# Performance work log

Measured on AMD Instinct MI355X. Metric: run time of the kernel, lower is better.

The kernel has to match this reference:

```python
import jax, jax.numpy as jnp
import numpy as np

N, M, D = 8192, 8192, 256

def setup_inputs() -> dict:
    key = jax.random.key(0)
    ks = jax.random.split(key, 8)
    s = 1.0 / np.sqrt(D)
    return {
        "x_q": jax.random.normal(ks[0], (N, D), dtype=jnp.float32),
        "x_kv": jax.random.normal(ks[1], (M, D), dtype=jnp.float32),
        "Wq": jax.random.uniform(ks[2], (D, D), minval=-s, maxval=s, dtype=jnp.float32),
        "bq": jax.random.uniform(ks[3], (D,), minval=-s, maxval=s, dtype=jnp.float32),
        "Wk": jax.random.uniform(ks[4], (D, D), minval=-s, maxval=s, dtype=jnp.float32),
        "bk": jax.random.uniform(ks[5], (D,), minval=-s, maxval=s, dtype=jnp.float32),
        "Wv": jax.random.uniform(ks[6], (D, D), minval=-s, maxval=s, dtype=jnp.float32),
        "bv": jax.random.uniform(ks[7], (D,), minval=-s, maxval=s, dtype=jnp.float32),
    }

def reference(x_q, x_kv, Wq, bq, Wk, bk, Wv, bv):
    # Linear layers: y = x @ W^T + b (torch convention: W is [out, in])
    q = x_q @ Wq.T + bq          # [N, D]
    k = x_kv @ Wk.T + bk         # [M, D]
    v = x_kv @ Wv.T + bv         # [M, D]
    scale = jnp.sqrt(jnp.asarray(q.shape[1], q.dtype))
    attn = jnp.einsum('nd,md->nm', q, k) / scale  # [N, M]
    attn = jax.nn.softmax(attn, axis=1)
    return attn @ v              # [N, D]
```

## Files before the change

### kernel.cpp

```cpp
#include <hip/hip_runtime.h>

#define NN 8192
#define MM 8192
#define DD 256
#define NPART 8
#define MPART (MM / NPART)
#define BK 64
#define NT (MPART / BK)
#define QT 32

#define SCALE_C 0.0901684403f
#define RAW_THR 127.5f

typedef short bf16x8 __attribute__((ext_vector_type(8)));
typedef float f32x4 __attribute__((ext_vector_type(4)));
typedef float f32x16 __attribute__((ext_vector_type(16)));
typedef unsigned int u32;
typedef u32 u32x2 __attribute__((ext_vector_type(2)));
typedef u32 u32x4 __attribute__((ext_vector_type(4)));

#define GLL16(src, dst) __builtin_amdgcn_global_load_lds( \
    (__attribute__((address_space(1))) void*)(src), \
    (__attribute__((address_space(3))) void*)(dst), 16, 0, 0)

static __device__ __forceinline__ unsigned char f2fp8(float a) {
    u32 r;
    asm("v_cvt_pk_fp8_f32 %0, %1, %1" : "=v"(r) : "v"(a));
    return (unsigned char)(r & 0xFFu);
}

static __device__ __forceinline__ u32 cvtpk(float lo, float hi) {
    u32 r;
    asm("v_cvt_pk_bf16_f32 %0, %1, %2" : "=v"(r) : "v"(lo), "v"(hi));
    return r;
}

static __device__ __forceinline__ float bf2f(short s) {
    return __builtin_bit_cast(float, (u32)((unsigned short)s) << 16);
}

__global__ __launch_bounds__(256, 2) void proj_kernel(
    const float* __restrict__ xq, const float* __restrict__ xkv,
    const float* __restrict__ Wq, const float* __restrict__ bq,
    const float* __restrict__ Wk, const float* __restrict__ bk,
    const float* __restrict__ Wv, const float* __restrict__ bv,
    unsigned char* __restrict__ q8, unsigned char* __restrict__ k8,
    short* __restrict__ vp)
{
    __shared__ short Xs[64][264];
    __shared__ short Ws[64][264];

    const int bid = blockIdx.x;
    const int iskv = bid >> 9;
    const int t = bid & 511;
    const int rt = t >> 2;
    const int ct = t & 3;
    const float* __restrict__ X = iskv ? xkv : xq;
    const float* __restrict__ W1 = iskv ? Wk : Wq;

    const int tid = threadIdx.x;
    const int lane = tid & 63;
    const int wv = tid >> 6;
    const int l15 = lane & 15;
    const int lg = lane >> 4;

    #pragma unroll
    for (int i = 0; i < 16; ++i) {
        int c = i * 256 + tid;
        int row = c >> 6;
        int col4 = (c & 63) << 2;
        f32x4 xv = *reinterpret_cast<const f32x4*>(X + (size_t)(rt * 64 + row) * DD + col4);
        f32x4 wr = *reinterpret_cast<const f32x4*>(W1 + (size_t)(ct * 64 + row) * DD + col4);
        u32x2 xb, wb;
        xb[0] = cvtpk(xv[0], xv[1]); xb[1] = cvtpk(xv[2], xv[3]);
        wb[0] = cvtpk(wr[0], wr[1]); wb[1] = cvtpk(wr[2], wr[3]);
        *reinterpret_cast<u32x2*>(&Xs[row][col4]) = xb;
        *reinterpret_cast<u32x2*>(&Ws[row][col4]) = wb;
    }
    __syncthreads();

    f32x4 acc[4];
    #pragma unroll
    for (int f = 0; f < 4; ++f) acc[f] = f32x4{0.f, 0.f, 0.f, 0.f};

    #pragma unroll
    for (int kk = 0; kk < 8; ++kk) {
        bf16x8 a = *reinterpret_cast<const bf16x8*>(&Xs[wv * 16 + l15][kk * 32 + lg * 8]);
        #pragma unroll
        for (int f = 0; f < 4; ++f) {
            bf16x8 b = *reinterpret_cast<const bf16x8*>(&Ws[f * 16 + l15][kk * 32 + lg * 8]);
            acc[f] = __builtin_amdgcn_mfma_f32_16x16x32_bf16(a, b, acc[f], 0, 0, 0);
        }
    }

    if (!iskv) {
        #pragma unroll
        for (int f = 0; f < 4; ++f) {
            const int o = ct * 64 + f * 16 + l15;
            const float bsv = bq[o];
            #pragma unroll
            for (int r = 0; r < 4; ++r) {
                const int rowg = rt * 64 + wv * 16 + lg * 4 + r;
                q8[(size_t)rowg * DD + o] = f2fp8(acc[f][r] + bsv);
            }
        }
        return;
    }

    #pragma unroll
    for (int f = 0; f < 4; ++f) {
        const int o = ct * 64 + f * 16 + l15;
        const float bsv = bk[o];
        #pragma unroll
        for (int r = 0; r < 4; ++r) {
            const int rowg = rt * 64 + wv * 16 + lg * 4 + r;
            k8[(size_t)(o >> 3) * (MM * 8) + (size_t)rowg * 8 + (o & 7)] = f2fp8(acc[f][r] + bsv);
        }
    }

    __syncthreads();
    #pragma unroll
    for (int i = 0; i < 16; ++i) {
        int c = i * 256 + tid;
        int row = c >> 6;
        int col4 = (c & 63) << 2;
        f32x4 wr = *reinterpret_cast<const f32x4*>(Wv + (size_t)(ct * 64 + row) * DD + col4);
        u32x2 wb;
        wb[0] = cvtpk(wr[0], wr[1]); wb[1] = cvtpk(wr[2], wr[3]);
        *reinterpret_cast<u32x2*>(&Ws[row][col4]) = wb;
    }
    __syncthreads();

    #pragma unroll
    for (int f = 0; f < 4; ++f) acc[f] = f32x4{0.f, 0.f, 0.f, 0.f};
    #pragma unroll
    for (int kk = 0; kk < 8; ++kk) {
        bf16x8 a = *reinterpret_cast<const bf16x8*>(&Xs[wv * 16 + l15][kk * 32 + lg * 8]);
        #pragma unroll
        for (int f = 0; f < 4; ++f) {
            bf16x8 b = *reinterpret_cast<const bf16x8*>(&Ws[f * 16 + l15][kk * 32 + lg * 8]);
            acc[f] = __builtin_amdgcn_mfma_f32_16x16x32_bf16(a, b, acc[f], 0, 0, 0);
        }
    }
    #pragma unroll
    for (int f = 0; f < 4; ++f) {
        const int o = ct * 64 + f * 16 + l15;
        const float bsv = bv[o];
        const int mb = rt * 64 + wv * 16 + lg * 4;
        u32 w0 = cvtpk(acc[f][0] + bsv, acc[f][1] + bsv);
        u32 w1 = cvtpk(acc[f][2] + bsv, acc[f][3] + bsv);
        u32x2 pk; pk[0] = w0; pk[1] = w1;
        *reinterpret_cast<u32x2*>(&vp[(size_t)(mb >> 6) * 16384 + o * 64 + (mb & 63)]) = pk;
    }
}

__global__ __launch_bounds__(512, 2) void attn_kernel(
    const unsigned char* __restrict__ qg, const unsigned char* __restrict__ kg,
    const short* __restrict__ vp, short* __restrict__ outpB,
    float* __restrict__ statm, float* __restrict__ statl)
{
    extern __shared__ short lds[];
    short* KsBase = lds;
    short* VsBase = lds + 3 * 8192;

    const int bid = blockIdx.x;
    const int p = bid & 7;
    const int qt = bid >> 3;
    const int q0 = qt * 256;
    const int tile0 = p * NT;

    const int tid = threadIdx.x;
    const int lane = tid & 63;
    const int w = tid >> 6;
    const int l31 = lane & 31;
    const int h = lane >> 5;

    long qf8[16];
    {
        const unsigned char* qr = qg + (size_t)(q0 + w * 32 + l31) * DD + h * 8;
        #pragma unroll
        for (int kt = 0; kt < 16; ++kt)
            qf8[kt] = __builtin_bit_cast(long, *reinterpret_cast<const u32x2*>(qr + kt * 16));
    }

    int koff[2], jdstK[2], voff[4], jdstV[4];
    #pragma unroll
    for (int i = 0; i < 2; ++i) {
        const int j = w * 2 + i;
        const int pl = 2 * j + (lane >> 5);
        koff[i] = pl * (MM * 8) + (lane & 31) * 16;
        jdstK[i] = __builtin_amdgcn_readfirstlane(j * 512);
    }
    #pragma unroll
    for (int i = 0; i < 4; ++i) {
        const int j = w * 4 + i;
        const int d = j * 8 + (lane >> 3);
        const int cl = ((lane & 7) - (d & 7)) & 7;
        voff[i] = d * 64 + (cl << 3);
        jdstV[i] = __builtin_amdgcn_readfirstlane(j * 512);
    }

    f32x16 o[8];
    #pragma unroll
    for (int dt = 0; dt < 8; ++dt)
        #pragma unroll
        for (int i = 0; i < 16; ++i) o[dt][i] = 0.f;
    float mrun = -1e30f, lrun = 0.f;

    #pragma unroll
    for (int i = 0; i < 2; ++i)
        GLL16(kg + (size_t)tile0 * 512 + koff[i], KsBase + jdstK[i]);
    #pragma unroll
    for (int i = 0; i < 4; ++i)
        GLL16(vp + (size_t)tile0 * 16384 + voff[i], VsBase + jdstV[i]);
    #pragma unroll
    for (int i = 0; i < 2; ++i)
        GLL16(kg + (size_t)(tile0 + 1) * 512 + koff[i], KsBase + 8192 + jdstK[i]);
    asm volatile("s_waitcnt vmcnt(2)\n\ts_barrier" ::: "memory");

    int kR = 0, kN = 1, kW = 2;
    #pragma unroll 1
    for (int t = 0; t < NT; ++t) {
        const char* kb = (const char*)(KsBase + kR * 8192);
        const char* vb = (const char*)(VsBase + (t & 1) * 16384);

        if (t + 1 < NT) {
            const size_t tb = (size_t)(tile0 + t + 1) * 16384;
            short* vd = VsBase + ((t + 1) & 1) * 16384;
            #pragma unroll
            for (int i = 0; i < 4; ++i) GLL16(vp + tb + voff[i], vd + jdstV[i]);
        }
        if (t + 2 < NT) {
            const size_t tb = (size_t)(tile0 + t + 2) * 512;
            short* kd = KsBase + kW * 8192;
            #pragma unroll
            for (int i = 0; i < 2; ++i) GLL16(kg + tb + koff[i], kd + jdstK[i]);
        }

        f32x16 sL, sH;
        #pragma unroll
        for (int i = 0; i < 16; ++i) { sL[i] = 0.f; sH[i] = 0.f; }
        __builtin_amdgcn_s_setprio(1);
        #pragma unroll
        for (int kt = 0; kt < 16; ++kt) {
            const int gb = (kt * 2 + h) * 512 + l31 * 8;
            long aL = __builtin_bit_cast(long, *reinterpret_cast<const u32x2*>(kb + gb));
            long aH = __builtin_bit_cast(long, *reinterpret_cast<const u32x2*>(kb + gb + 256));
            sL = __builtin_amdgcn_mfma_f32_32x32x16_fp8_fp8(aL, qf8[kt], sL, 0, 0, 0);
            sH = __builtin_amdgcn_mfma_f32_32x32x16_fp8_fp8(aH, qf8[kt], sH, 0, 0, 0);
        }
        __builtin_amdgcn_s_setprio(0);

        float mx;
        {
            float a0 = fmaxf(fmaxf(sL[0], sL[1]), fmaxf(sL[2], sL[3]));
            float a1 = fmaxf(fmaxf(sL[4], sL[5]), fmaxf(sL[6], sL[7]));
            float a2 = fmaxf(fmaxf(sL[8], sL[9]), fmaxf(sL[10], sL[11]));
            float a3 = fmaxf(fmaxf(sL[12], sL[13]), fmaxf(sL[14], sL[15]));
            float b0 = fmaxf(fmaxf(sH[0], sH[1]), fmaxf(sH[2], sH[3]));
            float b1 = fmaxf(fmaxf(sH[4], sH[5]), fmaxf(sH[6], sH[7]));
            float b2 = fmaxf(fmaxf(sH[8], sH[9]), fmaxf(sH[10], sH[11]));
            float b3 = fmaxf(fmaxf(sH[12], sH[13]), fmaxf(sH[14], sH[15]));
            mx = fmaxf(fmaxf(fmaxf(a0, a1), fmaxf(a2, a3)),
                       fmaxf(fmaxf(b0, b1), fmaxf(b2, b3)));
            mx = fmaxf(mx, __shfl_xor(mx, 32));
        }
        if (__any(mx > mrun + RAW_THR)) {
            const float mn = fmaxf(mrun, mx);
            const float al = __builtin_amdgcn_exp2f((mrun - mn) * SCALE_C);
            mrun = mn;
            lrun *= al;
            #pragma unroll
            for (int dt = 0; dt < 8; ++dt)
                #pragma unroll
                for (int i = 0; i < 16; ++i) o[dt][i] *= al;
        }
        const float msc = -mrun * SCALE_C;
        #pragma unroll
        for (int i = 0; i < 16; ++i) {
            sL[i] = __builtin_amdgcn_exp2f(fmaf(sL[i], SCALE_C, msc));
            sH[i] = __builtin_amdgcn_exp2f(fmaf(sH[i], SCALE_C, msc));
        }
        {
            float r0 = ((sL[0] + sL[1]) + (sL[2] + sL[3])) + ((sL[4] + sL[5]) + (sL[6] + sL[7]));
            float r1 = ((sL[8] + sL[9]) + (sL[10] + sL[11])) + ((sL[12] + sL[13]) + (sL[14] + sL[15]));
            float r2 = ((sH[0] + sH[1]) + (sH[2] + sH[3])) + ((sH[4] + sH[5]) + (sH[6] + sH[7]));
            float r3 = ((sH[8] + sH[9]) + (sH[10] + sH[11])) + ((sH[12] + sH[13]) + (sH[14] + sH[15]));
            float rs = (r0 + r1) + (r2 + r3);
            rs += __shfl_xor(rs, 32);
            lrun += rs;
        }

        bf16x8 pb[4];
        #pragma unroll
        for (int half = 0; half < 2; ++half) {
            const f32x16& sv = half ? sH : sL;
            #pragma unroll
            for (int g = 0; g < 2; ++g) {
                u32 pa = cvtpk(sv[g * 8 + 0], sv[g * 8 + 1]);
                u32 pbq = cvtpk(sv[g * 8 + 2], sv[g * 8 + 3]);
                u32 pc = cvtpk(sv[g * 8 + 4], sv[g * 8 + 5]);
                u32 pd = cvtpk(sv[g * 8 + 6], sv[g * 8 + 7]);
                const u32 xa = (u32)__shfl_xor((int)pa, 32);
                const u32 xb = (u32)__shfl_xor((int)pbq, 32);
                const u32 xc = (u32)__shfl_xor((int)pc, 32);
                const u32 xd = (u32)__shfl_xor((int)pd, 32);
                u32x4 bb;
                bb[0] = h ? xc : pa;
                bb[1] = h ? xd : pbq;
                bb[2] = h ? pc : xa;
                bb[3] = h ? pd : xb;
                pb[half * 2 + g] = __builtin_bit_cast(bf16x8, bb);
            }
        }

        __builtin_amdgcn_s_setprio(1);
        #pragma unroll
        for (int dt = 0; dt < 8; ++dt) {
            const int d = dt * 32 + l31;
            const char* rbase = vb + d * 128;
            const int rot = d & 7;
            bf16x8 a0 = *reinterpret_cast<const bf16x8*>(rbase + (((0 + h + rot) & 7) << 4));
            bf16x8 a1 = *reinterpret_cast<const bf16x8*>(rbase + (((2 + h + rot) & 7) << 4));
            bf16x8 a2 = *reinterpret_cast<const bf16x8*>(rbase + (((4 + h + rot) & 7) << 4));
            bf16x8 a3 = *reinterpret_cast<const bf16x8*>(rbase + (((6 + h + rot) & 7) << 4));
            o[dt] = __builtin_amdgcn_mfma_f32_32x32x16_bf16(a0, pb[0], o[dt], 0, 0, 0);
            o[dt] = __builtin_amdgcn_mfma_f32_32x32x16_bf16(a1, pb[1], o[dt], 0, 0, 0);
            o[dt] = __builtin_amdgcn_mfma_f32_32x32x16_bf16(a2, pb[2], o[dt], 0, 0, 0);
            o[dt] = __builtin_amdgcn_mfma_f32_32x32x16_bf16(a3, pb[3], o[dt], 0, 0, 0);
        }
        __builtin_amdgcn_s_setprio(0);

        if (t + 2 < NT) {
            asm volatile("s_waitcnt vmcnt(2)\n\ts_barrier" ::: "memory");
        } else if (t + 1 < NT) {
            asm volatile("s_waitcnt vmcnt(0)\n\ts_barrier" ::: "memory");
        }
        const int tmp = kR; kR = kN; kN = kW; kW = tmp;
    }

    const int qc = q0 + w * 32 + l31;
    #pragma unroll
    for (int dt = 0; dt < 8; ++dt) {
        #pragma unroll
        for (int i = 0; i < 16; i += 2) {
            const u32 two = cvtpk(o[dt][i], o[dt][i + 1]);
            const int dg = dt * 32 + (i & 3) + 8 * (i >> 2) + 4 * h;
            outpB[((size_t)p * DD + dg) * NN + qc] = (short)(two & 0xFFFFu);
            outpB[((size_t)p * DD + dg + 1) * NN + qc] = (short)(two >> 16);
        }
    }
    if (h == 0) {
        statm[(size_t)p * NN + qc] = mrun;
        statl[(size_t)p * NN + qc] = lrun;
    }
}

__global__ __launch_bounds__(256) void combine_kernel(
    const short* __restrict__ outpB, const float* __restrict__ statm,
    const float* __restrict__ statl, float* __restrict__ out)
{
    __shared__ float Wn[NPART][QT];
    __shared__ float Ot[QT][DD + 4];

    const int q0 = blockIdx.x * QT;
    const int tid = threadIdx.x;

    if (tid < QT) {
        const int q = q0 + tid;
        float mv[NPART], lv[NPART];
        float mM = -1e30f;
        #pragma unroll
        for (int p = 0; p < NPART; ++p) {
            mv[p] = statm[(size_t)p * NN + q];
            lv[p] = statl[(size_t)p * NN + q];
            mM = fmaxf(mM, mv[p]);
        }
        float L = 0.f;
        float wg[NPART];
        #pragma unroll
        for (int p = 0; p < NPART; ++p) {
            wg[p] = exp2f((mv[p] - mM) * SCALE_C);
            L += wg[p] * lv[p];
        }
        const float inv = 1.0f / L;
        #pragma unroll
        for (int p = 0; p < NPART; ++p) Wn[p][tid] = wg[p] * inv;
    }
    __syncthreads();

    {
        const int q = tid & 31;
        const int ds = tid >> 5;
        #pragma unroll 4
        for (int d = ds; d < DD; d += 8) {
            float acc = 0.f;
            #pragma unroll
            for (int p = 0; p < NPART; ++p)
                acc += Wn[p][q] * bf2f(outpB[((size_t)p * DD + d) * NN + q0 + q]);
            Ot[q][d] = acc;
        }
    }
    __syncthreads();

    {
        const int qq = tid >> 3;
        const int c = tid & 7;
        #pragma unroll
        for (int j = 0; j < 8; ++j) {
            const int d = c * 32 + j * 4;
            *reinterpret_cast<f32x4*>(&out[(size_t)(q0 + qq) * DD + d]) =
                *reinterpret_cast<const f32x4*>(&Ot[qq][d]);
        }
    }
}

extern "C" void kernel_launch(void* const* d_in, const int* in_sizes, int n_in,
                              void* d_out, int out_size, void* d_ws, size_t ws_size,
                              hipStream_t stream) {
    const float* xq  = (const float*)d_in[0];
    const float* xkv = (const float*)d_in[1];
    const float* Wq  = (const float*)d_in[2];
    const float* bq  = (const float*)d_in[3];
    const float* Wk  = (const float*)d_in[4];
    const float* bk  = (const float*)d_in[5];
    const float* Wv  = (const float*)d_in[6];
    const float* bv  = (const float*)d_in[7];
    float* out = (float*)d_out;

    char* ws = (char*)d_ws;
    unsigned char* qb8 = (unsigned char*)(ws);
    unsigned char* kb8 = (unsigned char*)(ws + ((size_t)4 << 20));
    short* vpb = (short*)(ws + ((size_t)8 << 20));
    short* outpB = (short*)(ws + ((size_t)12 << 20));
    float* sm = (float*)(ws + ((size_t)12 << 20) + (size_t)NPART * NN * DD * 2);
    float* sl = sm + (size_t)NPART * NN;

    hipFuncSetAttribute(reinterpret_cast<const void*>(attn_kernel),
                        hipFuncAttributeMaxDynamicSharedMemorySize, 114688);

    proj_kernel<<<1024, 256, 0, stream>>>(xq, xkv, Wq, bq, Wk, bk, Wv, bv, qb8, kb8, vpb);
    attn_kernel<<<256, 512, 114688, stream>>>(qb8, kb8, vpb, outpB, sm, sl);
    combine_kernel<<<NN / QT, 256, 0, stream>>>(outpB, sm, sl, out);
}
```

Before: 101.6 us.

## Software-pipeline QK and PV MFMAs across tiles with triple-buffered V

Restructures the attention loop so the P·V MFMAs of the previous tile are interleaved with the Q·K MFMAs of the current tile. This adds a peeled prologue and epilogue and moves V to triple buffering, with K buffers reused on a rotating schedule. Dynamic LDS grows from 114688 to 147456 bytes, which may reduce occupancy from two blocks per CU. The combine kernel is also reworked to handle 64 queries per 1024-thread block with paired bf16 loads.

```diff
diff --git a/kernel.cpp b/kernel.cpp
--- a/kernel.cpp
+++ b/kernel.cpp
@@ -7,7 +7,6 @@
 #define MPART (MM / NPART)
 #define BK 64
 #define NT (MPART / BK)
-#define QT 32
 
 #define SCALE_C 0.0901684403f
 #define RAW_THR 127.5f
@@ -147,9 +146,9 @@
         const int o = ct * 64 + f * 16 + l15;
         const float bsv = bv[o];
         const int mb = rt * 64 + wv * 16 + lg * 4;
-        u32 w0 = cvtpk(acc[f][0] + bsv, acc[f][1] + bsv);
-        u32 w1 = cvtpk(acc[f][2] + bsv, acc[f][3] + bsv);
-        u32x2 pk; pk[0] = w0; pk[1] = w1;
+        u32x2 pk;
+        pk[0] = cvtpk(acc[f][0] + bsv, acc[f][1] + bsv);
+        pk[1] = cvtpk(acc[f][2] + bsv, acc[f][3] + bsv);
         *reinterpret_cast<u32x2*>(&vp[(size_t)(mb >> 6) * 16384 + o * 64 + (mb & 63)]) = pk;
     }
 }
@@ -206,6 +205,7 @@
         #pragma unroll
         for (int i = 0; i < 16; ++i) o[dt][i] = 0.f;
     float mrun = -1e30f, lrun = 0.f;
+    bf16x8 pb[4];
 
     #pragma unroll
     for (int i = 0; i < 2; ++i)
@@ -216,26 +216,16 @@
     #pragma unroll
     for (int i = 0; i < 2; ++i)
         GLL16(kg + (size_t)(tile0 + 1) * 512 + koff[i], KsBase + 8192 + jdstK[i]);
-    asm volatile("s_waitcnt vmcnt(2)\n\ts_barrier" ::: "memory");
-
-    int kR = 0, kN = 1, kW = 2;
-    #pragma unroll 1
-    for (int t = 0; t < NT; ++t) {
-        const char* kb = (const char*)(KsBase + kR * 8192);
-        const char* vb = (const char*)(VsBase + (t & 1) * 16384);
-
-        if (t + 1 < NT) {
-            const size_t tb = (size_t)(tile0 + t + 1) * 16384;
-            short* vd = VsBase + ((t + 1) & 1) * 16384;
-            #pragma unroll
-            for (int i = 0; i < 4; ++i) GLL16(vp + tb + voff[i], vd + jdstV[i]);
-        }
-        if (t + 2 < NT) {
-            const size_t tb = (size_t)(tile0 + t + 2) * 512;
-            short* kd = KsBase + kW * 8192;
-            #pragma unroll
-            for (int i = 0; i < 2; ++i) GLL16(kg + tb + koff[i], kd + jdstK[i]);
-        }
+    asm volatile("s_waitcnt vmcnt(6)\n\ts_barrier" ::: "memory");
+
+    {
+        const char* kb = (const char*)KsBase;
+        #pragma unroll
+        for (int i = 0; i < 4; ++i)
+            GLL16(vp + (size_t)(tile0 + 1) * 16384 + voff[i], VsBase + 16384 + jdstV[i]);
+        #pragma unroll
+        for (int i = 0; i < 2; ++i)
+            GLL16(kg + (size_t)(tile0 + 2) * 512 + koff[i], KsBase + 2 * 8192 + jdstK[i]);
 
         f32x16 sL, sH;
         #pragma unroll
@@ -265,16 +255,7 @@
                        fmaxf(fmaxf(b0, b1), fmaxf(b2, b3)));
             mx = fmaxf(mx, __shfl_xor(mx, 32));
         }
-        if (__any(mx > mrun + RAW_THR)) {
-            const float mn = fmaxf(mrun, mx);
-            const float al = __builtin_amdgcn_exp2f((mrun - mn) * SCALE_C);
-            mrun = mn;
-            lrun *= al;
-            #pragma unroll
-            for (int dt = 0; dt < 8; ++dt)
-                #pragma unroll
-                for (int i = 0; i < 16; ++i) o[dt][i] *= al;
-        }
+        mrun = mx;
         const float msc = -mrun * SCALE_C;
         #pragma unroll
         for (int i = 0; i < 16; ++i) {
@@ -290,8 +271,6 @@
             rs += __shfl_xor(rs, 32);
             lrun += rs;
         }
-
-        bf16x8 pb[4];
         #pragma unroll
         for (int half = 0; half < 2; ++half) {
             const f32x16& sv = half ? sH : sL;
@@ -313,7 +292,133 @@
                 pb[half * 2 + g] = __builtin_bit_cast(bf16x8, bb);
             }
         }
-
+        asm volatile("s_waitcnt vmcnt(6)\n\ts_barrier" ::: "memory");
+    }
+
+    int cur = 1;
+    #pragma unroll 1
+    for (int t = 1; t < NT; ++t) {
+        const char* kb = (const char*)(KsBase + cur * 8192);
+        const int vprev = (cur == 0) ? 2 : cur - 1;
+        const char* vbp = (const char*)(VsBase + vprev * 16384);
+
+        if (t + 1 < NT) {
+            const int vw = (cur == 2) ? 0 : cur + 1;
+            const size_t tb = (size_t)(tile0 + t + 1) * 16384;
+            short* vd = VsBase + vw * 16384;
+            #pragma unroll
+            for (int i = 0; i < 4; ++i) GLL16(vp + tb + voff[i], vd + jdstV[i]);
+        }
+        if (t + 2 < NT) {
+            const size_t tb = (size_t)(tile0 + t + 2) * 512;
+            short* kd = KsBase + vprev * 8192;
+            #pragma unroll
+            for (int i = 0; i < 2; ++i) GLL16(kg + tb + koff[i], kd + jdstK[i]);
+        }
+
+        f32x16 sL, sH;
+        #pragma unroll
+        for (int i = 0; i < 16; ++i) { sL[i] = 0.f; sH[i] = 0.f; }
+        __builtin_amdgcn_s_setprio(1);
+        #pragma unroll
+        for (int kt = 0; kt < 16; ++kt) {
+            const int gb = (kt * 2 + h) * 512 + l31 * 8;
+            long aL = __builtin_bit_cast(long, *reinterpret_cast<const u32x2*>(kb + gb));
+            long aH = __builtin_bit_cast(long, *reinterpret_cast<const u32x2*>(kb + gb + 256));
+            sL = __builtin_amdgcn_mfma_f32_32x32x16_fp8_fp8(aL, qf8[kt], sL, 0, 0, 0);
+            sH = __builtin_amdgcn_mfma_f32_32x32x16_fp8_fp8(aH, qf8[kt], sH, 0, 0, 0);
+            {
+                const int j = 2 * kt;
+                const int dt = j & 7, ks = j >> 3;
+                const int d = dt * 32 + l31;
+                bf16x8 av = *reinterpret_cast<const bf16x8*>(
+                    vbp + d * 128 + (((2 * ks + h + (d & 7)) & 7) << 4));
+                o[dt] = __builtin_amdgcn_mfma_f32_32x32x16_bf16(av, pb[ks], o[dt], 0, 0, 0);
+            }
+            {
+                const int j = 2 * kt + 1;
+                const int dt = j & 7, ks = j >> 3;
+                const int d = dt * 32 + l31;
+                bf16x8 av = *reinterpret_cast<const bf16x8*>(
+                    vbp + d * 128 + (((2 * ks + h + (d & 7)) & 7) << 4));
+                o[dt] = __builtin_amdgcn_mfma_f32_32x32x16_bf16(av, pb[ks], o[dt], 0, 0, 0);
+            }
+        }
+        __builtin_amdgcn_s_setprio(0);
+
+        float mx;
+        {
+            float a0 = fmaxf(fmaxf(sL[0], sL[1]), fmaxf(sL[2], sL[3]));
+            float a1 = fmaxf(fmaxf(sL[4], sL[5]), fmaxf(sL[6], sL[7]));
+            float a2 = fmaxf(fmaxf(sL[8], sL[9]), fmaxf(sL[10], sL[11]));
+            float a3 = fmaxf(fmaxf(sL[12], sL[13]), fmaxf(sL[14], sL[15]));
+            float b0 = fmaxf(fmaxf(sH[0], sH[1]), fmaxf(sH[2], sH[3]));
+            float b1 = fmaxf(fmaxf(sH[4], sH[5]), fmaxf(sH[6], sH[7]));
+            float b2 = fmaxf(fmaxf(sH[8], sH[9]), fmaxf(sH[10], sH[11]));
+            float b3 = fmaxf(fmaxf(sH[12], sH[13]), fmaxf(sH[14], sH[15]));
+            mx = fmaxf(fmaxf(fmaxf(a0, a1), fmaxf(a2, a3)),
+                       fmaxf(fmaxf(b0, b1), fmaxf(b2, b3)));
+            mx = fmaxf(mx, __shfl_xor(mx, 32));
+        }
+        if (__any(mx > mrun + RAW_THR)) {
+            const float mn = fmaxf(mrun, mx);
+            const float al = __builtin_amdgcn_exp2f((mrun - mn) * SCALE_C);
+            mrun = mn;
+            lrun *= al;
+            #pragma unroll
+            for (int dt = 0; dt < 8; ++dt)
+                #pragma unroll
+                for (int i = 0; i < 16; ++i) o[dt][i] *= al;
+        }
+        const float msc = -mrun * SCALE_C;
+        #pragma unroll
+        for (int i = 0; i < 16; ++i) {
+            sL[i] = __builtin_amdgcn_exp2f(fmaf(sL[i], SCALE_C, msc));
+            sH[i] = __builtin_amdgcn_exp2f(fmaf(sH[i], SCALE_C, msc));
+        }
+        {
+            float r0 = ((sL[0] + sL[1]) + (sL[2] + sL[3])) + ((sL[4] + sL[5]) + (sL[6] + sL[7]));
+            float r1 = ((sL[8] + sL[9]) + (sL[10] + sL[11])) + ((sL[12] + sL[13]) + (sL[14] + sL[15]));
+            float r2 = ((sH[0] + sH[1]) + (sH[2] + sH[3])) + ((sH[4] + sH[5]) + (sH[6] + sH[7]));
+            float r3 = ((sH[8] + sH[9]) + (sH[10] + sH[11])) + ((sH[12] + sH[13]) + (sH[14] + sH[15]));
+            float rs = (r0 + r1) + (r2 + r3);
+            rs += __shfl_xor(rs, 32);
+            lrun += rs;
+        }
+        #pragma unroll
+        for (int half = 0; half < 2; ++half) {
+            const f32x16& sv = half ? sH : sL;
+            #pragma unroll
+            for (int g = 0; g < 2; ++g) {
+                u32 pa = cvtpk(sv[g * 8 + 0], sv[g * 8 + 1]);
+                u32 pbq = cvtpk(sv[g * 8 + 2], sv[g * 8 + 3]);
+                u32 pc = cvtpk(sv[g * 8 + 4], sv[g * 8 + 5]);
+                u32 pd = cvtpk(sv[g * 8 + 6], sv[g * 8 + 7]);
+                const u32 xa = (u32)__shfl_xor((int)pa, 32);
+                const u32 xb = (u32)__shfl_xor((int)pbq, 32);
+                const u32 xc = (u32)__shfl_xor((int)pc, 32);
+                const u32 xd = (u32)__shfl_xor((int)pd, 32);
+                u32x4 bb;
+                bb[0] = h ? xc : pa;
+                bb[1] = h ? xd : pbq;
+                bb[2] = h ? pc : xa;
+                bb[3] = h ? pd : xb;
+                pb[half * 2 + g] = __builtin_bit_cast(bf16x8, bb);
+            }
+        }
+
+        if (t + 2 < NT) {
+            asm volatile("s_waitcnt vmcnt(6)\n\ts_barrier" ::: "memory");
+        } else if (t + 1 < NT) {
+            asm volatile("s_waitcnt vmcnt(4)\n\ts_barrier" ::: "memory");
+        } else {
+            asm volatile("s_waitcnt vmcnt(0)\n\ts_barrier" ::: "memory");
+        }
+        cur = (cur == 2) ? 0 : cur + 1;
+    }
+
+    {
+        const char* vb = (const char*)(VsBase + ((NT - 1) % 3) * 16384);
         __builtin_amdgcn_s_setprio(1);
         #pragma unroll
         for (int dt = 0; dt < 8; ++dt) {
@@ -330,13 +435,6 @@
             o[dt] = __builtin_amdgcn_mfma_f32_32x32x16_bf16(a3, pb[3], o[dt], 0, 0, 0);
         }
         __builtin_amdgcn_s_setprio(0);
-
-        if (t + 2 < NT) {
-            asm volatile("s_waitcnt vmcnt(2)\n\ts_barrier" ::: "memory");
-        } else if (t + 1 < NT) {
-            asm volatile("s_waitcnt vmcnt(0)\n\ts_barrier" ::: "memory");
-        }
-        const int tmp = kR; kR = kN; kN = kW; kW = tmp;
     }
 
     const int qc = q0 + w * 32 + l31;
@@ -356,17 +454,17 @@
     }
 }
 
-__global__ __launch_bounds__(256) void combine_kernel(
+__global__ __launch_bounds__(1024) void combine_kernel(
     const short* __restrict__ outpB, const float* __restrict__ statm,
     const float* __restrict__ statl, float* __restrict__ out)
 {
-    __shared__ float Wn[NPART][QT];
-    __shared__ float Ot[QT][DD + 4];
-
-    const int q0 = blockIdx.x * QT;
+    __shared__ float Wn[NPART][64];
+    __shared__ float Ot[64][DD + 2];
+
+    const int q0 = blockIdx.x * 64;
     const int tid = threadIdx.x;
 
-    if (tid < QT) {
+    if (tid < 64) {
         const int q = q0 + tid;
         float mv[NPART], lv[NPART];
         float mM = -1e30f;
@@ -390,25 +488,32 @@
     __syncthreads();
 
     {
-        const int q = tid & 31;
-        const int ds = tid >> 5;
-        #pragma unroll 4
-        for (int d = ds; d < DD; d += 8) {
-            float acc = 0.f;
-            #pragma unroll
-            for (int p = 0; p < NPART; ++p)
-                acc += Wn[p][q] * bf2f(outpB[((size_t)p * DD + d) * NN + q0 + q]);
-            Ot[q][d] = acc;
+        const int pr = tid & 31;
+        const int d0 = tid >> 5;
+        const float w0 = Wn[0][pr * 2], w0b = Wn[0][pr * 2 + 1];
+        (void)w0; (void)w0b;
+        #pragma unroll 2
+        for (int d = d0; d < DD; d += 32) {
+            float a0 = 0.f, a1 = 0.f;
+            #pragma unroll
+            for (int p = 0; p < NPART; ++p) {
+                const u32 two = *reinterpret_cast<const u32*>(
+                    &outpB[((size_t)p * DD + d) * NN + q0 + pr * 2]);
+                a0 += Wn[p][pr * 2] * __builtin_bit_cast(float, two << 16);
+                a1 += Wn[p][pr * 2 + 1] * __builtin_bit_cast(float, two & 0xFFFF0000u);
+            }
+            Ot[pr * 2][d] = a0;
+            Ot[pr * 2 + 1][d] = a1;
         }
     }
     __syncthreads();
 
     {
-        const int qq = tid >> 3;
-        const int c = tid & 7;
-        #pragma unroll
-        for (int j = 0; j < 8; ++j) {
-            const int d = c * 32 + j * 4;
+        const int qq = tid >> 4;
+        const int c = tid & 15;
+        #pragma unroll
+        for (int j = 0; j < 4; ++j) {
+            const int d = c * 16 + j * 4;
             *reinterpret_cast<f32x4*>(&out[(size_t)(q0 + qq) * DD + d]) =
                 *reinterpret_cast<const f32x4*>(&Ot[qq][d]);
         }
@@ -437,9 +542,9 @@
     float* sl = sm + (size_t)NPART * NN;
 
     hipFuncSetAttribute(reinterpret_cast<const void*>(attn_kernel),
-                        hipFuncAttributeMaxDynamicSharedMemorySize, 114688);
+                        hipFuncAttributeMaxDynamicSharedMemorySize, 147456);
 
     proj_kernel<<<1024, 256, 0, stream>>>(xq, xkv, Wq, bq, Wk, bk, Wv, bv, qb8, kb8, vpb);
-    attn_kernel<<<256, 512, 114688, stream>>>(qb8, kb8, vpb, outpB, sm, sl);
-    combine_kernel<<<NN / QT, 256, 0, stream>>>(outpB, sm, sl, out);
-}
+    attn_kernel<<<256, 512, 147456, stream>>>(qb8, kb8, vpb, outpB, sm, sl);
+    combine_kernel<<<NN / 64, 1024, 0, stream>>>(outpB, sm, sl, out);
+}
```

Measured after the change: 97.27 us. -4.3%, faster.
